# Optimization experiments

Hardware: AMD Instinct MI355X
Metric: run time of the kernel (lower is better)

Reference implementation:

```python
import jax, jax.numpy as jnp
import numpy as np
from jax import lax

B, LATENT, SEQ, HID, OUT = 4096, 128, 512, 32, 64


def setup_inputs() -> dict:
    key = jax.random.key(0)
    ks = jax.random.split(key, 9)
    s = 1.0 / np.sqrt(HID)  # PyTorch-style init scale
    f32 = jnp.float32
    return {
        "z": jax.random.normal(ks[0], (B, LATENT), f32),
        "init_W": jax.random.uniform(ks[1], (HID, LATENT), f32, -s, s),
        "init_b": jax.random.uniform(ks[2], (HID,), f32, -s, s),
        "W_ih": jax.random.uniform(ks[3], (4 * HID, HID), f32, -s, s),
        "W_hh": jax.random.uniform(ks[4], (4 * HID, HID), f32, -s, s),
        "b_ih": jax.random.uniform(ks[5], (4 * HID,), f32, -s, s),
        "b_hh": jax.random.uniform(ks[6], (4 * HID,), f32, -s, s),
        "out_W": jax.random.uniform(ks[7], (OUT, HID), f32, -s, s),
        "out_b": jax.random.uniform(ks[8], (OUT,), f32, -s, s),
    }


def reference(z, init_W, init_b, W_ih, W_hh, b_ih, b_hh, out_W, out_b):
    # init_fc: z -> h0 (num_layers=1); cell starts at zero
    h0 = z @ init_W.T + init_b  # [B, H]
    c0 = jnp.zeros_like(h0)

    # x_in is all zeros, so the input-to-hidden term is a constant bias;
    # compute it once (keeps W_ih in the graph, matmul with zeros == 0).
    x_zero = jnp.zeros((z.shape[0], W_ih.shape[1]), z.dtype)
    gate_const = x_zero @ W_ih.T + b_ih + b_hh  # [B, 4H]

    def step(carry, _):
        h, c = carry
        gates = h @ W_hh.T + gate_const  # [B, 4H], PyTorch gate order i,f,g,o
        i, f, g, o = jnp.split(gates, 4, axis=-1)
        i = jax.nn.sigmoid(i)
        f = jax.nn.sigmoid(f)
        g = jnp.tanh(g)
        o = jax.nn.sigmoid(o)
        c = f * c + i * g
        h = o * jnp.tanh(c)
        return (h, c), h

    _, hs = lax.scan(step, (h0, c0), None, length=SEQ)  # [T, B, H]
    out = jnp.transpose(hs, (1, 0, 2))  # [B, T, H] (batch_first)
    y = out @ out_W.T + out_b  # [B, T, OUT]
    return y
```

## Files before the change

### kernel.cpp

```cpp
#include <hip/hip_runtime.h>


#define B_SZ   4096
#define LATENT 128
#define SEQ    512
#define HID    32
#define OUT_N  64
#define ROWS   16
#define LSW    40
#define HXW    10

typedef _Float16 f16x8 __attribute__((ext_vector_type(8)));
typedef _Float16 f16x4 __attribute__((ext_vector_type(4)));
typedef float    f32x4 __attribute__((ext_vector_type(4)));

__device__ __forceinline__ float fexp2(float x) { return __builtin_amdgcn_exp2f(x); }
__device__ __forceinline__ float frcp(float x)  { return __builtin_amdgcn_rcpf(x); }
__device__ __forceinline__ void lds_barrier() {
    asm volatile("s_waitcnt lgkmcnt(0)\n\ts_barrier" ::: "memory");
}

__global__ __launch_bounds__(512)
void lstm_tr16(const float* __restrict__ z,
               const float* __restrict__ init_W,
               const float* __restrict__ init_b,
               const float* __restrict__ W_hh,
               const float* __restrict__ b_ih,
               const float* __restrict__ b_hh,
               const float* __restrict__ out_W,
               const float* __restrict__ out_b,
               float* __restrict__ y)
{
    __shared__ __align__(16) _Float16 hst[ROWS * LSW];
    __shared__ __align__(4) unsigned short hx[2][64][HXW];

    const int tid  = threadIdx.x;
    const int w    = tid >> 6;
    const int lane = tid & 63;
    const int n_   = lane & 15;
    const int kb   = lane >> 4;
    const int jj   = w & 1;
    const int r_   = w >> 1;
    const int rbase = blockIdx.x * ROWS;

    const float NL2E  = -1.44269504088896341f;
    const float P2L2E =  2.88539008177792681f;

    f16x8 wf1;
    f32x4 bacc1;
    {
        const int arow = 32 * (n_ & 3) + 16 * jj + 4 * (n_ >> 2) + r_;
        const float asc = ((n_ & 3) == 2) ? P2L2E : NL2E;
        const float* wrow = W_hh + (size_t)arow * HID;
#pragma unroll
        for (int rr = 0; rr < 4; rr++) {
            wf1[rr]     = (_Float16)(asc * wrow[4 * kb + rr]);
            wf1[4 + rr] = (_Float16)(asc * wrow[16 + 4 * kb + rr]);
        }
#pragma unroll
        for (int r = 0; r < 4; r++) {
            const int G = 32 * r + 16 * jj + 4 * kb + r_;
            const float bsc = (r == 2) ? P2L2E : NL2E;
            bacc1[r] = bsc * (b_ih[G] + b_hh[G]);
        }
    }

    f16x8 owf;
    f32x4 oacc;
    {
        const int p = r_;
        const float* row = out_W + (size_t)(16 * p + n_) * HID;
#pragma unroll
        for (int rr = 0; rr < 4; rr++) {
            owf[rr]     = (_Float16)row[4 * kb + rr];
            owf[4 + rr] = (_Float16)row[4 * kb + 16 + rr];
        }
#pragma unroll
        for (int r = 0; r < 4; r++) oacc[r] = out_b[16 * p + 4 * kb + r];
    }

    {
        int m = tid >> 5, j = tid & 31;
        const float4* zp = (const float4*)(z + (size_t)(rbase + m) * LATENT);
        const float4* wp = (const float4*)(init_W + (size_t)j * LATENT);
        float acc = init_b[j];
#pragma unroll
        for (int k = 0; k < LATENT / 4; k++) {
            float4 a4 = zp[k], b4 = wp[k];
            acc = fmaf(a4.x, b4.x, acc); acc = fmaf(a4.y, b4.y, acc);
            acc = fmaf(a4.z, b4.z, acc); acc = fmaf(a4.w, b4.w, acc);
        }
        hst[m * LSW + j] = (_Float16)acc;
    }
    __syncthreads();

    f16x8 a;
    {
        f16x4 lo = *(const f16x4*)&hst[n_ * LSW + 4 * kb];
        f16x4 hi = *(const f16x4*)&hst[n_ * LSW + 4 * kb + 16];
#pragma unroll
        for (int r = 0; r < 4; r++) { a[r] = lo[r]; a[4 + r] = hi[r]; }
    }

    float cs = 0.f;

    float* yb = y + (size_t)(rbase + n_) * SEQ * OUT_N + 16 * r_ + 4 * kb;

    for (int t = 0; t < SEQ; t += 4) {
#pragma unroll
        for (int u = 0; u < 4; u++) {
            const int par = u & 1;
            f32x4 acc = __builtin_amdgcn_mfma_f32_16x16x32_f16(wf1, a, bacc1, 0, 0, 0);

            if (jj == par) {
                f32x4 py = __builtin_amdgcn_mfma_f32_16x16x32_f16(owf, a, oacc, 0, 0, 0);
                if (t + u) *(f32x4*)(yb + (size_t)(t + u - 1) * OUT_N) = py;
            }

            {
                float Fi  = fexp2(acc[0]);
                float Ff  = fexp2(acc[1]);
                float Eg  = fexp2(acc[2]);
                float Fo  = fexp2(acc[3]);
                float rig = frcp((1.f + Fi) * (1.f + Eg));
                float tg  = fmaf(P2L2E, Eg, -P2L2E);
                float ig  = tg * rig;
                float gf  = frcp(1.f + Ff);
                float csn = fmaf(gf, cs, ig);
                cs = csn;
                float Ecs = fexp2(fminf(csn, 126.f));
                float rd  = frcp((1.f + Fo) * (1.f + Ecs));
                float hh  = (Ecs - 1.f) * rd;
                union { _Float16 h; unsigned short u16; } cv;
                cv.h = (_Float16)hh;
                hx[par][lane][4 * jj + r_] = cv.u16;
            }
            lds_barrier();

            {
                union { unsigned uu[4]; f16x8 v; } ua;
                const unsigned* rp = (const unsigned*)&hx[par][lane][0];
                ua.uu[0] = rp[0]; ua.uu[1] = rp[1]; ua.uu[2] = rp[2]; ua.uu[3] = rp[3];
                a = ua.v;
            }
        }
    }

    if (jj == 0) {
        f32x4 py = __builtin_amdgcn_mfma_f32_16x16x32_f16(owf, a, oacc, 0, 0, 0);
        *(f32x4*)(yb + (size_t)(SEQ - 1) * OUT_N) = py;
    }
}

extern "C" void kernel_launch(void* const* d_in, const int* in_sizes, int n_in,
                              void* d_out, int out_size, void* d_ws, size_t ws_size,
                              hipStream_t stream) {
    const float* z      = (const float*)d_in[0];
    const float* init_W = (const float*)d_in[1];
    const float* init_b = (const float*)d_in[2];
    const float* W_hh   = (const float*)d_in[4];
    const float* b_ih   = (const float*)d_in[5];
    const float* b_hh   = (const float*)d_in[6];
    const float* out_W  = (const float*)d_in[7];
    const float* out_b  = (const float*)d_in[8];
    float* yout = (float*)d_out;

    lstm_tr16<<<B_SZ / ROWS, 512, 0, stream>>>(z, init_W, init_b, W_hh, b_ih, b_hh,
                                               out_W, out_b, yout);
}
```

Baseline: 578.3 us.

## Halve LSTM block to 4 waves, each computing two hidden units per step

The recurrent kernel now launches 4 waves per 16-row block instead of 8. Each wave issues two gate MFMAs and evaluates two hidden units per lane, then writes both as one packed 32-bit LDS store. Every wave now also runs the output projection MFMA each step instead of half the waves. The aim is to cut barrier participants and per-step synchronization cost and to use wider LDS stores, in exchange for a longer per-wave serial chain of MFMAs and transcendentals within each timestep.

```diff
diff --git a/kernel.cpp b/kernel.cpp
--- a/kernel.cpp
+++ b/kernel.cpp
@@ -8,7 +8,7 @@
 #define OUT_N  64
 #define ROWS   16
 #define LSW    40
-#define HXW    10
+#define HXD    5
 
 typedef _Float16 f16x8 __attribute__((ext_vector_type(8)));
 typedef _Float16 f16x4 __attribute__((ext_vector_type(4)));
@@ -20,133 +20,157 @@
     asm volatile("s_waitcnt lgkmcnt(0)\n\ts_barrier" ::: "memory");
 }
 
-__global__ __launch_bounds__(512)
-void lstm_tr16(const float* __restrict__ z,
-               const float* __restrict__ init_W,
-               const float* __restrict__ init_b,
-               const float* __restrict__ W_hh,
-               const float* __restrict__ b_ih,
-               const float* __restrict__ b_hh,
-               const float* __restrict__ out_W,
-               const float* __restrict__ out_b,
-               float* __restrict__ y)
+__global__ __launch_bounds__(256)
+void lstm_q17(const float* __restrict__ z,
+              const float* __restrict__ init_W,
+              const float* __restrict__ init_b,
+              const float* __restrict__ W_hh,
+              const float* __restrict__ b_ih,
+              const float* __restrict__ b_hh,
+              const float* __restrict__ out_W,
+              const float* __restrict__ out_b,
+              float* __restrict__ y)
 {
     __shared__ __align__(16) _Float16 hst[ROWS * LSW];
-    __shared__ __align__(4) unsigned short hx[2][64][HXW];
+    __shared__ __align__(4) unsigned hx[2][64][HXD];
 
     const int tid  = threadIdx.x;
     const int w    = tid >> 6;
     const int lane = tid & 63;
     const int n_   = lane & 15;
-    const int kb   = lane >> 4;
-    const int jj   = w & 1;
-    const int r_   = w >> 1;
+    const int q    = lane >> 4;
+    const int s_   = w >> 1;
+    const int p0   = w & 1;
     const int rbase = blockIdx.x * ROWS;
 
     const float NL2E  = -1.44269504088896341f;
     const float P2L2E =  2.88539008177792681f;
 
-    f16x8 wf1;
-    f32x4 bacc1;
-    {
-        const int arow = 32 * (n_ & 3) + 16 * jj + 4 * (n_ >> 2) + r_;
+    f16x8 wf0, wf1;
+    f32x4 bacc0, bacc1;
+#pragma unroll
+    for (int m = 0; m < 2; m++) {
+        const int arow = 32 * (n_ & 3) + 16 * s_ + 4 * (n_ >> 2) + 2 * p0 + m;
         const float asc = ((n_ & 3) == 2) ? P2L2E : NL2E;
         const float* wrow = W_hh + (size_t)arow * HID;
+        f16x8 v;
 #pragma unroll
         for (int rr = 0; rr < 4; rr++) {
-            wf1[rr]     = (_Float16)(asc * wrow[4 * kb + rr]);
-            wf1[4 + rr] = (_Float16)(asc * wrow[16 + 4 * kb + rr]);
+            v[rr]     = (_Float16)(asc * wrow[4 * q + rr]);
+            v[4 + rr] = (_Float16)(asc * wrow[16 + 4 * q + rr]);
         }
+        f32x4 b;
 #pragma unroll
         for (int r = 0; r < 4; r++) {
-            const int G = 32 * r + 16 * jj + 4 * kb + r_;
+            const int G = 32 * r + 16 * s_ + 4 * q + 2 * p0 + m;
             const float bsc = (r == 2) ? P2L2E : NL2E;
-            bacc1[r] = bsc * (b_ih[G] + b_hh[G]);
+            b[r] = bsc * (b_ih[G] + b_hh[G]);
         }
+        if (m == 0) { wf0 = v; bacc0 = b; } else { wf1 = v; bacc1 = b; }
     }
 
     f16x8 owf;
     f32x4 oacc;
     {
-        const int p = r_;
+        const int p = w;
         const float* row = out_W + (size_t)(16 * p + n_) * HID;
 #pragma unroll
         for (int rr = 0; rr < 4; rr++) {
-            owf[rr]     = (_Float16)row[4 * kb + rr];
-            owf[4 + rr] = (_Float16)row[4 * kb + 16 + rr];
+            owf[rr]     = (_Float16)row[4 * q + rr];
+            owf[4 + rr] = (_Float16)row[16 + 4 * q + rr];
         }
 #pragma unroll
-        for (int r = 0; r < 4; r++) oacc[r] = out_b[16 * p + 4 * kb + r];
+        for (int r = 0; r < 4; r++) oacc[r] = out_b[16 * p + 4 * q + r];
     }
 
     {
-        int m = tid >> 5, j = tid & 31;
+        int m = tid >> 4, j0 = tid & 15;
         const float4* zp = (const float4*)(z + (size_t)(rbase + m) * LATENT);
-        const float4* wp = (const float4*)(init_W + (size_t)j * LATENT);
-        float acc = init_b[j];
 #pragma unroll
-        for (int k = 0; k < LATENT / 4; k++) {
-            float4 a4 = zp[k], b4 = wp[k];
-            acc = fmaf(a4.x, b4.x, acc); acc = fmaf(a4.y, b4.y, acc);
-            acc = fmaf(a4.z, b4.z, acc); acc = fmaf(a4.w, b4.w, acc);
+        for (int half = 0; half < 2; half++) {
+            const int j = j0 + 16 * half;
+            const float4* wp = (const float4*)(init_W + (size_t)j * LATENT);
+            float acc = init_b[j];
+#pragma unroll
+            for (int k = 0; k < LATENT / 4; k++) {
+                float4 a4 = zp[k], b4 = wp[k];
+                acc = fmaf(a4.x, b4.x, acc); acc = fmaf(a4.y, b4.y, acc);
+                acc = fmaf(a4.z, b4.z, acc); acc = fmaf(a4.w, b4.w, acc);
+            }
+            hst[m * LSW + j] = (_Float16)acc;
         }
-        hst[m * LSW + j] = (_Float16)acc;
     }
     __syncthreads();
 
     f16x8 a;
     {
-        f16x4 lo = *(const f16x4*)&hst[n_ * LSW + 4 * kb];
-        f16x4 hi = *(const f16x4*)&hst[n_ * LSW + 4 * kb + 16];
+        f16x4 lo = *(const f16x4*)&hst[n_ * LSW + 4 * q];
+        f16x4 hi = *(const f16x4*)&hst[n_ * LSW + 4 * q + 16];
 #pragma unroll
         for (int r = 0; r < 4; r++) { a[r] = lo[r]; a[4 + r] = hi[r]; }
     }
 
-    float cs = 0.f;
+    float cs0 = 0.f, cs1 = 0.f;
 
-    float* yb = y + (size_t)(rbase + n_) * SEQ * OUT_N + 16 * r_ + 4 * kb;
+    float* yb = y + (size_t)(rbase + n_) * SEQ * OUT_N + 16 * w + 4 * q;
 
     for (int t = 0; t < SEQ; t += 4) {
 #pragma unroll
         for (int u = 0; u < 4; u++) {
             const int par = u & 1;
-            f32x4 acc = __builtin_amdgcn_mfma_f32_16x16x32_f16(wf1, a, bacc1, 0, 0, 0);
+            f32x4 ac0 = __builtin_amdgcn_mfma_f32_16x16x32_f16(wf0, a, bacc0, 0, 0, 0);
+            f32x4 ac1 = __builtin_amdgcn_mfma_f32_16x16x32_f16(wf1, a, bacc1, 0, 0, 0);
 
-            if (jj == par) {
+            {
                 f32x4 py = __builtin_amdgcn_mfma_f32_16x16x32_f16(owf, a, oacc, 0, 0, 0);
                 if (t + u) *(f32x4*)(yb + (size_t)(t + u - 1) * OUT_N) = py;
             }
 
+            union { _Float16 h[2]; unsigned u32; } cv;
             {
-                float Fi  = fexp2(acc[0]);
-                float Ff  = fexp2(acc[1]);
-                float Eg  = fexp2(acc[2]);
-                float Fo  = fexp2(acc[3]);
+                float Fi  = fexp2(ac0[0]);
+                float Ff  = fexp2(ac0[1]);
+                float Eg  = fexp2(ac0[2]);
+                float Fo  = fexp2(ac0[3]);
                 float rig = frcp((1.f + Fi) * (1.f + Eg));
                 float tg  = fmaf(P2L2E, Eg, -P2L2E);
                 float ig  = tg * rig;
                 float gf  = frcp(1.f + Ff);
-                float csn = fmaf(gf, cs, ig);
-                cs = csn;
+                float csn = fmaf(gf, cs0, ig);
+                cs0 = csn;
                 float Ecs = fexp2(fminf(csn, 126.f));
                 float rd  = frcp((1.f + Fo) * (1.f + Ecs));
-                float hh  = (Ecs - 1.f) * rd;
-                union { _Float16 h; unsigned short u16; } cv;
-                cv.h = (_Float16)hh;
-                hx[par][lane][4 * jj + r_] = cv.u16;
+                cv.h[0] = (_Float16)((Ecs - 1.f) * rd);
             }
+            {
+                float Fi  = fexp2(ac1[0]);
+                float Ff  = fexp2(ac1[1]);
+                float Eg  = fexp2(ac1[2]);
+                float Fo  = fexp2(ac1[3]);
+                float rig = frcp((1.f + Fi) * (1.f + Eg));
+                float tg  = fmaf(P2L2E, Eg, -P2L2E);
+                float ig  = tg * rig;
+                float gf  = frcp(1.f + Ff);
+                float csn = fmaf(gf, cs1, ig);
+                cs1 = csn;
+                float Ecs = fexp2(fminf(csn, 126.f));
+                float rd  = frcp((1.f + Fo) * (1.f + Ecs));
+                cv.h[1] = (_Float16)((Ecs - 1.f) * rd);
+            }
+            hx[par][lane][w] = cv.u32;
+
             lds_barrier();
 
             {
                 union { unsigned uu[4]; f16x8 v; } ua;
-                const unsigned* rp = (const unsigned*)&hx[par][lane][0];
+                const unsigned* rp = &hx[par][lane][0];
                 ua.uu[0] = rp[0]; ua.uu[1] = rp[1]; ua.uu[2] = rp[2]; ua.uu[3] = rp[3];
                 a = ua.v;
             }
         }
     }
 
-    if (jj == 0) {
+    {
         f32x4 py = __builtin_amdgcn_mfma_f32_16x16x32_f16(owf, a, oacc, 0, 0, 0);
         *(f32x4*)(yb + (size_t)(SEQ - 1) * OUT_N) = py;
     }
@@ -165,6 +189,6 @@
     const float* out_b  = (const float*)d_in[8];
     float* yout = (float*)d_out;
 
-    lstm_tr16<<<B_SZ / ROWS, 512, 0, stream>>>(z, init_W, init_b, W_hh, b_ih, b_hh,
-                                               out_W, out_b, yout);
+    lstm_q17<<<B_SZ / ROWS, 256, 0, stream>>>(z, init_W, init_b, W_hh, b_ih, b_hh,
+                                              out_W, out_b, yout);
 }
```

New measurement: 630.3 us. 1.09x slower.
